# Kernel tuning notes

Measured on AMD Instinct MI355X. Metric: run time of the kernel, lower is better.

## Reference

```python
import jax, jax.numpy as jnp
import numpy as np

D_IN = 1024
D_OUT = 1024


def setup_inputs() -> dict:
    key = jax.random.key(0)
    kx, kq, kk, kv = jax.random.split(key, 4)
    x = jax.random.normal(kx, (4, 2048, D_IN), dtype=jnp.float32)
    s = 1.0 / np.sqrt(D_IN)
    Wq = jax.random.normal(kq, (D_IN, D_OUT), dtype=jnp.float32) * s
    Wk = jax.random.normal(kk, (D_IN, D_OUT), dtype=jnp.float32) * s
    Wv = jax.random.normal(kv, (D_IN, D_OUT), dtype=jnp.float32) * s
    return {"x": x, "Wq": Wq, "Wk": Wk, "Wv": Wv}


def reference(x, Wq, Wk, Wv):
    # x: [B, S, d_in]; W*: [d_in, d_out]
    B, S, _ = x.shape
    q = x @ Wq  # [B, S, d_out]
    k = x @ Wk
    v = x @ Wv
    scale = 1.0 / jnp.sqrt(jnp.asarray(k.shape[-1], x.dtype))
    scores = jnp.einsum("bqd,bkd->bqk", q, k) * scale  # [B, S, S]
    # causal mask: positions j > i masked to -inf (triu, diagonal=1)
    causal = jnp.tril(jnp.ones((S, S), dtype=bool))
    scores = jnp.where(causal[None, :, :], scores, -jnp.inf)
    attn = jax.nn.softmax(scores, axis=-1)  # dropout p=0.0 -> identity
    return jnp.einsum("bqk,bkd->bqd", attn, v)
```

## Files before the change

### kernel.cpp

```cpp
#include <hip/hip_runtime.h>
#include <hip/hip_bf16.h>

#define NB 4
#define SB 2048
#define DD 1024
#define BM 128
#define BN 128
#define BK 32

typedef __attribute__((ext_vector_type(8))) short bf16x8;
typedef __attribute__((ext_vector_type(4))) short bf16x4;
typedef __attribute__((ext_vector_type(4))) float f32x4;
typedef unsigned int u32;

__device__ __forceinline__ float bf2f(unsigned short u) {
    return __uint_as_float(((u32)u) << 16);
}
__device__ __forceinline__ short f2bf(float f) {
    u32 u = __float_as_uint(f);
    u32 r = (u + 0x7fffu + ((u >> 16) & 1u)) >> 16;
    return (short)r;
}

__device__ __forceinline__ void wait_vm8() {
    asm volatile("s_waitcnt vmcnt(8)" ::: "memory");
}
__device__ __forceinline__ void wait_vm0() {
    asm volatile("s_waitcnt vmcnt(0)" ::: "memory");
}
__device__ __forceinline__ void barrier_raw() {
    __builtin_amdgcn_s_barrier();
    asm volatile("" ::: "memory");
}

__device__ __forceinline__ void mfma_step(const short* As, const short* Bs,
                                          f32x4 (&acc)[4][4], int lane, int wave)
{
    const int wm = (wave >> 1) * 64, wn = (wave & 1) * 64;
    const int fr = lane & 15;
    const int quad = lane >> 4;
    bf16x8 af[4], bf[4];
#pragma unroll
    for (int t = 0; t < 4; t++) {
        af[t] = *(const bf16x8*)&As[(wm + t * 16 + fr) * BK + quad * 8];
        bf[t] = *(const bf16x8*)&Bs[(wn + t * 16 + fr) * BK + quad * 8];
    }
#pragma unroll
    for (int mt = 0; mt < 4; mt++)
#pragma unroll
        for (int nt = 0; nt < 4; nt++)
            acc[mt][nt] = __builtin_amdgcn_mfma_f32_16x16x32_bf16(
                af[mt], bf[nt], acc[mt][nt], 0, 0, 0);
}

__device__ __forceinline__ void mfma_step_swz(const short* As, const short* Bs,
                                              f32x4 (&acc)[4][4], int lane,
                                              int wave)
{
    const int wm = (wave >> 1) * 64, wn = (wave & 1) * 64;
    const int fr = lane & 15;
    const int qa = (lane >> 4) ^ ((fr >> 1) & 3);
    bf16x8 af[4], bf[4];
#pragma unroll
    for (int t = 0; t < 4; t++) {
        af[t] = *(const bf16x8*)&As[(wm + t * 16 + fr) * BK + qa * 8];
        bf[t] = *(const bf16x8*)&Bs[(wn + t * 16 + fr) * BK + qa * 8];
    }
#pragma unroll
    for (int mt = 0; mt < 4; mt++)
#pragma unroll
        for (int nt = 0; nt < 4; nt++)
            acc[mt][nt] = __builtin_amdgcn_mfma_f32_16x16x32_bf16(
                af[mt], bf[nt], acc[mt][nt], 0, 0, 0);
}

__device__ __forceinline__ void mfma_step_pv_swz(const short* As,
                                                 const short* Bs,
                                                 f32x4 (&acc)[2][4], int lane,
                                                 int wave)
{
    const int wm = wave * 32;
    const int fr = lane & 15;
    const int qa = (lane >> 4) ^ ((fr >> 1) & 3);
    bf16x8 af[2], bf[4];
#pragma unroll
    for (int t = 0; t < 2; t++)
        af[t] = *(const bf16x8*)&As[(wm + t * 16 + fr) * BK + qa * 8];
#pragma unroll
    for (int t = 0; t < 4; t++)
        bf[t] = *(const bf16x8*)&Bs[(t * 16 + fr) * BK + qa * 8];
#pragma unroll
    for (int mt = 0; mt < 2; mt++)
#pragma unroll
        for (int nt = 0; nt < 4; nt++)
            acc[mt][nt] = __builtin_amdgcn_mfma_f32_16x16x32_bf16(
                af[mt], bf[nt], acc[mt][nt], 0, 0, 0);
}

__device__ __forceinline__ void mfma_step256_swz(const short* As,
                                                 const short* Bs,
                                                 f32x4 (&acc)[8][4], int lane,
                                                 int wave)
{
    const int wm = (wave >> 2) * 128;
    const int wn = (wave & 3) * 64;
    const int fr = lane & 15;
    const int qa = (lane >> 4) ^ ((fr >> 1) & 3);
    bf16x8 af[8], bf[4];
#pragma unroll
    for (int t = 0; t < 8; t++)
        af[t] = *(const bf16x8*)&As[(wm + t * 16 + fr) * BK + qa * 8];
#pragma unroll
    for (int t = 0; t < 4; t++)
        bf[t] = *(const bf16x8*)&Bs[(wn + t * 16 + fr) * BK + qa * 8];
#pragma unroll
    for (int mt = 0; mt < 8; mt++)
#pragma unroll
        for (int nt = 0; nt < 4; nt++)
            acc[mt][nt] = __builtin_amdgcn_mfma_f32_16x16x32_bf16(
                af[mt], bf[nt], acc[mt][nt], 0, 0, 0);
}

__device__ __forceinline__ void stage128x32(const short* __restrict__ g, int ld,
                                            short* lds, int tid) {
    const int wave = tid >> 6, lane = tid & 63;
    const int r = lane >> 2;
    const int c = ((lane & 3) ^ ((lane >> 3) & 3)) * 8;
#pragma unroll
    for (int i = 0; i < 2; i++) {
        const int chunk = wave * 2 + i;
        const short* gp = g + (size_t)(chunk * 16 + r) * ld + c;
        __builtin_amdgcn_global_load_lds(
            (const __attribute__((address_space(1))) u32*)gp,
            (__attribute__((address_space(3))) u32*)(lds + chunk * 512 + lane * 8),
            16, 0, 0);
    }
}

__device__ __forceinline__ void stage64x32(const short* __restrict__ g, int ld,
                                           short* lds, int tid) {
    const int wave = tid >> 6, lane = tid & 63;
    const int r = lane >> 2;
    const int c = ((lane & 3) ^ ((lane >> 3) & 3)) * 8;
    const short* gp = g + (size_t)(wave * 16 + r) * ld + c;
    __builtin_amdgcn_global_load_lds(
        (const __attribute__((address_space(1))) u32*)gp,
        (__attribute__((address_space(3))) u32*)(lds + wave * 512 + lane * 8),
        16, 0, 0);
}

__device__ __forceinline__ void stage256x64(const short* __restrict__ g, int ld,
                                            short* base, int tid) {
    const int w = tid >> 6, l = tid & 63;
    const int lr = l >> 2;
    const int lc = ((l & 3) ^ ((l >> 3) & 3)) * 8;
#pragma unroll
    for (int i = 0; i < 4; i++) {
        const int ks = i >> 1;
        const int row = (i & 1) * 128 + w * 16 + lr;
        const short* gp = g + (size_t)row * ld + ks * 32 + lc;
        __builtin_amdgcn_global_load_lds(
            (const __attribute__((address_space(1))) u32*)gp,
            (__attribute__((address_space(3))) u32*)(base + i * 4096 + w * 512 + l * 8),
            16, 0, 0);
    }
}

__device__ __forceinline__ void stage_f32_128x32(const float* __restrict__ g,
                                                 int ld, short* lds, int tid) {
    const int r = tid >> 1;
    const int c = (tid & 1) * 16;
    const float* gp = &g[(size_t)r * ld + c];
    float4 v0 = *(const float4*)(gp + 0);
    float4 v1 = *(const float4*)(gp + 4);
    float4 v2 = *(const float4*)(gp + 8);
    float4 v3 = *(const float4*)(gp + 12);
    bf16x8 o0, o1;
    o0[0] = f2bf(v0.x); o0[1] = f2bf(v0.y); o0[2] = f2bf(v0.z); o0[3] = f2bf(v0.w);
    o0[4] = f2bf(v1.x); o0[5] = f2bf(v1.y); o0[6] = f2bf(v1.z); o0[7] = f2bf(v1.w);
    o1[0] = f2bf(v2.x); o1[1] = f2bf(v2.y); o1[2] = f2bf(v2.z); o1[3] = f2bf(v2.w);
    o1[4] = f2bf(v3.x); o1[5] = f2bf(v3.y); o1[6] = f2bf(v3.z); o1[7] = f2bf(v3.w);
    *(bf16x8*)&lds[r * BK + c] = o0;
    *(bf16x8*)&lds[r * BK + c + 8] = o1;
}

__global__ __launch_bounds__(256) void prep_mm(
    const float* __restrict__ x, const float* __restrict__ Wq,
    const float* __restrict__ Wk, const float* __restrict__ Wv,
    short* __restrict__ xb, short* __restrict__ Wvt, float* __restrict__ Mp4)
{
    __shared__ short As[BM * BK], Bs[BN * BK];
    __shared__ short t[64][65];
    const int bx = blockIdx.x;
    const int tid = threadIdx.x;
    if (bx < 256) {
        const int ch = bx >> 6;
        const int t64 = bx & 63;
        const int m0 = (t64 >> 3) * BM;
        const int n0 = (t64 & 7) * BN;
        const int kbase = ch * 256;
        const int lane = tid & 63, wave = tid >> 6;
        f32x4 acc[4][4];
#pragma unroll
        for (int a = 0; a < 4; a++)
#pragma unroll
            for (int b = 0; b < 4; b++) acc[a][b] = (f32x4){0.f, 0.f, 0.f, 0.f};
        for (int k0 = 0; k0 < 256; k0 += BK) {
            stage_f32_128x32(Wk + (size_t)m0 * DD + kbase + k0, DD, As, tid);
            stage_f32_128x32(Wq + (size_t)n0 * DD + kbase + k0, DD, Bs, tid);
            __syncthreads();
            mfma_step(As, Bs, acc, lane, wave);
            __syncthreads();
        }
        const int wm = (wave >> 1) * 64, wn = (wave & 1) * 64;
        const int fr = lane & 15, quad = lane >> 4;
        float* Mc = Mp4 + (size_t)ch * DD * DD;
#pragma unroll
        for (int mt = 0; mt < 4; mt++)
#pragma unroll
            for (int nt = 0; nt < 4; nt++)
#pragma unroll
                for (int r = 0; r < 4; r++) {
                    const size_t m = m0 + wm + mt * 16 + quad * 4 + r;
                    const size_t n = n0 + wn + nt * 16 + fr;
                    Mc[m * DD + n] = acc[mt][nt][r];
                }
        return;
    }
    if (bx < 4352) {
        const size_t i = ((size_t)(bx - 256) * 256 + tid) * 8;
        float4 a = *(const float4*)&x[i];
        float4 b = *(const float4*)&x[i + 4];
        bf16x8 o;
        o[0] = f2bf(a.x); o[1] = f2bf(a.y); o[2] = f2bf(a.z); o[3] = f2bf(a.w);
        o[4] = f2bf(b.x); o[5] = f2bf(b.y); o[6] = f2bf(b.z); o[7] = f2bf(b.w);
        *(bf16x8*)&xb[i] = o;
        return;
    }
    const int rr = bx - 4352;
    const int k0 = (rr & 15) * 64;
    const int n0 = (rr >> 4) * 64;
    {
        const int r = tid >> 4;
        const int c = (tid & 15) * 4;
#pragma unroll
        for (int i = 0; i < 4; i++) {
            float4 v = *(const float4*)&Wv[(size_t)(k0 + i * 16 + r) * DD + n0 + c];
            t[i * 16 + r][c + 0] = f2bf(v.x);
            t[i * 16 + r][c + 1] = f2bf(v.y);
            t[i * 16 + r][c + 2] = f2bf(v.z);
            t[i * 16 + r][c + 3] = f2bf(v.w);
        }
    }
    __syncthreads();
    {
        const int r = tid >> 3;
        const int c = (tid & 7) * 8;
#pragma unroll
        for (int i = 0; i < 2; i++) {
            bf16x8 o;
#pragma unroll
            for (int j = 0; j < 8; j++) o[j] = t[c + j][i * 32 + r];
            *(bf16x8*)&Wvt[(size_t)(n0 + i * 32 + r) * DD + k0 + c] = o;
        }
    }
}

__global__ __launch_bounds__(256) void mm_reduce(const float* __restrict__ Mp4,
                                                 short* __restrict__ Mp)
{
    const size_t e = ((size_t)blockIdx.x * 256 + threadIdx.x) * 4;
    const size_t N = (size_t)DD * DD;
    float4 s = *(const float4*)&Mp4[e];
#pragma unroll
    for (int c = 1; c < 4; c++) {
        float4 p = *(const float4*)&Mp4[c * N + e];
        s.x += p.x; s.y += p.y; s.z += p.z; s.w += p.w;
    }
    bf16x4 o;
    o[0] = f2bf(s.x); o[1] = f2bf(s.y); o[2] = f2bf(s.z); o[3] = f2bf(s.w);
    *(bf16x4*)&Mp[e] = o;
}

__global__ __launch_bounds__(512) void tv_gemm(
    const short* __restrict__ xb, const short* __restrict__ Mp,
    const short* __restrict__ Wvt, short* __restrict__ T,
    short* __restrict__ Vt)
{
    __shared__ short lds[2 * 32768];
    const int lin = blockIdx.x + 4 * blockIdx.y;
    const int swz = (lin & 7) * 16 + (lin >> 3);
    const int n0 = (swz & 3) * 256;
    const int m0 = (swz >> 2) * 256;
    const int isv = blockIdx.z;
    const short* Bt = isv ? Wvt : Mp;
    const short* Ap = xb + (size_t)m0 * DD;
    const short* Bp = Bt + (size_t)n0 * DD;
    const int tid = threadIdx.x;
    const int lane = tid & 63, wave = tid >> 6;
    f32x4 acc[8][4];
#pragma unroll
    for (int a = 0; a < 8; a++)
#pragma unroll
        for (int b = 0; b < 4; b++) acc[a][b] = (f32x4){0.f, 0.f, 0.f, 0.f};

    stage256x64(Ap, DD, lds, tid);
    stage256x64(Bp, DD, lds + 16384, tid);
    for (int j = 0; j < 16; ++j) {
        const int cur = j & 1;
        short* slot = lds + cur * 32768;
        if (j < 15) {
            short* nxt = lds + (cur ^ 1) * 32768;
            stage256x64(Ap + (j + 1) * 64, DD, nxt, tid);
            stage256x64(Bp + (j + 1) * 64, DD, nxt + 16384, tid);
            wait_vm8();
        } else {
            wait_vm0();
        }
        barrier_raw();
        __builtin_amdgcn_s_setprio(1);
        mfma_step256_swz(slot, slot + 16384, acc, lane, wave);
        mfma_step256_swz(slot + 8192, slot + 16384 + 8192, acc, lane, wave);
        __builtin_amdgcn_s_setprio(0);
        barrier_raw();
    }

    const int wm = (wave >> 2) * 128, wn = (wave & 3) * 64;
    const int fr = lane & 15, quad = lane >> 4;
    if (!isv) {
#pragma unroll
        for (int mt = 0; mt < 8; mt++)
#pragma unroll
            for (int nt = 0; nt < 4; nt++)
#pragma unroll
                for (int r = 0; r < 4; r++) {
                    const size_t m = m0 + wm + mt * 16 + quad * 4 + r;
                    const size_t n = n0 + wn + nt * 16 + fr;
                    T[m * DD + n] = f2bf(acc[mt][nt][r]);
                }
    } else {
        const int bb = m0 >> 11;
        const int s0 = (m0 & (SB - 1)) + wm + quad * 4;
        short* Vb = Vt + (size_t)bb * DD * SB;
#pragma unroll
        for (int mt = 0; mt < 8; mt++)
#pragma unroll
            for (int nt = 0; nt < 4; nt++) {
                const size_t n = n0 + wn + nt * 16 + fr;
                const size_t s = s0 + mt * 16;
                bf16x4 o;
#pragma unroll
                for (int r = 0; r < 4; r++) o[r] = f2bf(acc[mt][nt][r]);
                *(bf16x4*)&Vb[n * SB + s] = o;
            }
    }
}

__global__ __launch_bounds__(256) void scores_mfma(
    const short* __restrict__ T, const short* __restrict__ xb,
    short* __restrict__ Sc)
{
    const int bx = blockIdx.x;
    const int idx = (bx & 7) * 34 + (bx >> 3);
    int qt = (int)((__fsqrt_rn(4.f * idx + 1.f) - 1.f) * 0.5f);
    while ((qt + 1) * (qt + 2) <= idx) qt++;
    while (qt * (qt + 1) > idx) qt--;
    const int kt = idx - qt * (qt + 1);
    const int qm0 = qt * BM;
    const int kn0 = kt * 64;
    const int b = blockIdx.y;
    __shared__ short As[2 * BM * BK], Bs[2 * 64 * BK];
    const short* Tq = T + (size_t)b * SB * DD + (size_t)qm0 * DD;
    const short* Xk = xb + (size_t)b * SB * DD + (size_t)kn0 * DD;
    short* Sb = Sc + (size_t)b * SB * SB;
    const int tid = threadIdx.x;
    const int lane = tid & 63, wave = tid >> 6;
    f32x4 acc[2][4];
#pragma unroll
    for (int a = 0; a < 2; a++)
#pragma unroll
        for (int c = 0; c < 4; c++) acc[a][c] = (f32x4){0.f, 0.f, 0.f, 0.f};
    for (int k0 = 0; k0 < DD; k0 += 2 * BK) {
        stage128x32(Tq + k0, DD, As, tid);
        stage128x32(Tq + k0 + BK, DD, As + BM * BK, tid);
        stage64x32(Xk + k0, DD, Bs, tid);
        stage64x32(Xk + k0 + BK, DD, Bs + 64 * BK, tid);
        __syncthreads();
        mfma_step_pv_swz(As, Bs, acc, lane, wave);
        mfma_step_pv_swz(As + BM * BK, Bs + 64 * BK, acc, lane, wave);
        __syncthreads();
    }
    const int fr = lane & 15, quad = lane >> 4;
    const float scale = 0.03125f;
#pragma unroll
    for (int mt = 0; mt < 2; mt++)
#pragma unroll
        for (int nt = 0; nt < 4; nt++)
#pragma unroll
            for (int r = 0; r < 4; r++) {
                const size_t q = qm0 + wave * 32 + mt * 16 + quad * 4 + r;
                const size_t k = kn0 + nt * 16 + fr;
                Sb[q * SB + k] = f2bf(acc[mt][nt][r] * scale);
            }
}

__global__ __launch_bounds__(256) void softmax_kernel(short* __restrict__ Sc)
{
    const int row = blockIdx.x;
    const int i = row & (SB - 1);
    const int jlim = ((i >> 7) + 1) << 7;
    short* r = Sc + (size_t)row * SB;
    const int t = threadIdx.x;
    const int lane = t & 63, wave = t >> 6;
    __shared__ float red[8];

    const int j0 = t * 8;
    bf16x8 in = {0, 0, 0, 0, 0, 0, 0, 0};
    if (j0 <= i) in = *(const bf16x8*)&r[j0];
    float v[8];
    float mx = -1e30f;
#pragma unroll
    for (int e = 0; e < 8; e++) {
        const float s = (j0 + e <= i) ? bf2f((unsigned short)in[e]) : -1e30f;
        v[e] = s;
        mx = fmaxf(mx, s);
    }
#pragma unroll
    for (int o = 32; o > 0; o >>= 1) mx = fmaxf(mx, __shfl_down(mx, o));
    if (lane == 0) red[wave] = mx;
    __syncthreads();
    mx = fmaxf(fmaxf(red[0], red[1]), fmaxf(red[2], red[3]));

    float sum = 0.f;
#pragma unroll
    for (int e = 0; e < 8; e++) {
        const float x = (j0 + e <= i) ? __expf(v[e] - mx) : 0.f;
        v[e] = x;
        sum += x;
    }
#pragma unroll
    for (int o = 32; o > 0; o >>= 1) sum += __shfl_down(sum, o);
    if (lane == 0) red[4 + wave] = sum;
    __syncthreads();
    const float inv = 1.0f / (red[4] + red[5] + red[6] + red[7]);
    if (j0 < jlim) {
        bf16x8 o;
#pragma unroll
        for (int e = 0; e < 8; e++) o[e] = f2bf(v[e] * inv);
        *(bf16x8*)&r[j0] = o;
    }
}

__global__ __launch_bounds__(256) void pv_mfma(
    const short* __restrict__ P, const short* __restrict__ Vt,
    float* __restrict__ O)
{
    __shared__ short As[2 * 8192], Bs[2 * 8192];
    const int pair = blockIdx.x;
    const int n0 = blockIdx.y * 128;
    const int b = blockIdx.z;
    const short* Pb = P + (size_t)b * SB * SB;
    const short* Vb = Vt + (size_t)b * DD * SB;
    float* Ob = O + (size_t)b * SB * DD;
    const int tid = threadIdx.x;
    const int lane = tid & 63, wave = tid >> 6;
    const int fr = lane & 15, quad = lane >> 4;
    for (int half = 0; half < 2; ++half) {
        const int qt = half ? (15 - pair) : pair;
        const int qm0 = qt * BM;
        const int nj = (qt + 1) * 2;
        const short* Pq = Pb + (size_t)qm0 * SB;
        const short* Vn = Vb + (size_t)n0 * SB;
        f32x4 acc[4][4];
#pragma unroll
        for (int a = 0; a < 4; a++)
#pragma unroll
            for (int c = 0; c < 4; c++) acc[a][c] = (f32x4){0.f, 0.f, 0.f, 0.f};
        stage128x32(Pq, SB, As, tid);
        stage128x32(Pq + BK, SB, As + 4096, tid);
        stage128x32(Vn, SB, Bs, tid);
        stage128x32(Vn + BK, SB, Bs + 4096, tid);
        for (int j = 0; j < nj; ++j) {
            const int cur = j & 1;
            const short* as = As + cur * 8192;
            const short* bs = Bs + cur * 8192;
            if (j + 1 < nj) {
                const int off = (j + 1) * 64;
                short* an = As + (cur ^ 1) * 8192;
                short* bn = Bs + (cur ^ 1) * 8192;
                stage128x32(Pq + off, SB, an, tid);
                stage128x32(Pq + off + BK, SB, an + 4096, tid);
                stage128x32(Vn + off, SB, bn, tid);
                stage128x32(Vn + off + BK, SB, bn + 4096, tid);
                wait_vm8();
            } else {
                wait_vm0();
            }
            barrier_raw();
            __builtin_amdgcn_s_setprio(1);
            mfma_step_swz(as, bs, acc, lane, wave);
            mfma_step_swz(as + 4096, bs + 4096, acc, lane, wave);
            __builtin_amdgcn_s_setprio(0);
            barrier_raw();
        }
        const int wm = (wave >> 1) * 64, wn = (wave & 1) * 64;
#pragma unroll
        for (int mt = 0; mt < 4; mt++)
#pragma unroll
            for (int nt = 0; nt < 4; nt++)
#pragma unroll
                for (int r = 0; r < 4; r++) {
                    const size_t q = qm0 + wm + mt * 16 + quad * 4 + r;
                    const size_t n = n0 + wn + nt * 16 + fr;
                    Ob[q * DD + n] = acc[mt][nt][r];
                }
    }
}

extern "C" void kernel_launch(void* const* d_in, const int* in_sizes, int n_in,
                              void* d_out, int out_size, void* d_ws, size_t ws_size,
                              hipStream_t stream)
{
    const float* x  = (const float*)d_in[0];
    const float* Wq = (const float*)d_in[1];
    const float* Wk = (const float*)d_in[2];
    const float* Wv = (const float*)d_in[3];
    float* out = (float*)d_out;

    const size_t XE = (size_t)NB * SB * DD;
    const size_t WE = (size_t)DD * DD;
    short* xb  = (short*)d_ws;
    short* T   = xb + XE;
    short* Vt  = T + XE;
    short* Sc  = Vt + XE;
    float* Pp  = (float*)(Sc + (size_t)NB * SB * SB);
    short* Wvt = (short*)(Pp + (size_t)NB * 1024 * DD);
    short* Mp  = Wvt + WE;
    float* Mp4 = (float*)Sc;

    prep_mm<<<dim3(256 + 4096 + 256), 256, 0, stream>>>(
        x, Wq, Wk, Wv, xb, Wvt, Mp4);
    mm_reduce<<<dim3(1024), 256, 0, stream>>>(Mp4, Mp);
    tv_gemm<<<dim3(4, 32, 2), 512, 0, stream>>>(xb, Mp, Wvt, T, Vt);
    scores_mfma<<<dim3(272, NB), 256, 0, stream>>>(T, xb, Sc);
    softmax_kernel<<<dim3(NB * SB), 256, 0, stream>>>(Sc);
    pv_mfma<<<dim3(8, 8, NB), 256, 0, stream>>>(Sc, Vt, out);
}
```

Baseline: 227.9 us.

## Use 128x128 tiles with double-buffered async staging in causal scores kernel

The scores kernel moves from 128x64 tiles over the lower-triangular block layout to 128x128 tiles, halving the grid and increasing reuse of each staged tile. It also replaces the synchronous load-then-compute loop with a double-buffered pipeline that prefetches the next 64-wide K slice while MFMAs run, using vmcnt waits, raw barriers and setprio. The cost is more LDS (64 KB) and more accumulator registers per block, plus fewer blocks to fill the machine. Diagonal tiles now compute a full 128x128 block, but the 128-aligned row limit in softmax already accounts for that.

```diff
diff --git a/kernel.cpp b/kernel.cpp
--- a/kernel.cpp
+++ b/kernel.cpp
@@ -68,29 +68,6 @@
     }
 #pragma unroll
     for (int mt = 0; mt < 4; mt++)
-#pragma unroll
-        for (int nt = 0; nt < 4; nt++)
-            acc[mt][nt] = __builtin_amdgcn_mfma_f32_16x16x32_bf16(
-                af[mt], bf[nt], acc[mt][nt], 0, 0, 0);
-}
-
-__device__ __forceinline__ void mfma_step_pv_swz(const short* As,
-                                                 const short* Bs,
-                                                 f32x4 (&acc)[2][4], int lane,
-                                                 int wave)
-{
-    const int wm = wave * 32;
-    const int fr = lane & 15;
-    const int qa = (lane >> 4) ^ ((fr >> 1) & 3);
-    bf16x8 af[2], bf[4];
-#pragma unroll
-    for (int t = 0; t < 2; t++)
-        af[t] = *(const bf16x8*)&As[(wm + t * 16 + fr) * BK + qa * 8];
-#pragma unroll
-    for (int t = 0; t < 4; t++)
-        bf[t] = *(const bf16x8*)&Bs[(t * 16 + fr) * BK + qa * 8];
-#pragma unroll
-    for (int mt = 0; mt < 2; mt++)
 #pragma unroll
         for (int nt = 0; nt < 4; nt++)
             acc[mt][nt] = __builtin_amdgcn_mfma_f32_16x16x32_bf16(
@@ -135,18 +112,6 @@
             (__attribute__((address_space(3))) u32*)(lds + chunk * 512 + lane * 8),
             16, 0, 0);
     }
-}
-
-__device__ __forceinline__ void stage64x32(const short* __restrict__ g, int ld,
-                                           short* lds, int tid) {
-    const int wave = tid >> 6, lane = tid & 63;
-    const int r = lane >> 2;
-    const int c = ((lane & 3) ^ ((lane >> 3) & 3)) * 8;
-    const short* gp = g + (size_t)(wave * 16 + r) * ld + c;
-    __builtin_amdgcn_global_load_lds(
-        (const __attribute__((address_space(1))) u32*)gp,
-        (__attribute__((address_space(3))) u32*)(lds + wave * 512 + lane * 8),
-        16, 0, 0);
 }
 
 __device__ __forceinline__ void stage256x64(const short* __restrict__ g, int ld,
@@ -360,46 +325,64 @@
     const short* __restrict__ T, const short* __restrict__ xb,
     short* __restrict__ Sc)
 {
+    __shared__ short As[2 * 8192], Bs[2 * 8192];
     const int bx = blockIdx.x;
-    const int idx = (bx & 7) * 34 + (bx >> 3);
-    int qt = (int)((__fsqrt_rn(4.f * idx + 1.f) - 1.f) * 0.5f);
-    while ((qt + 1) * (qt + 2) <= idx) qt++;
-    while (qt * (qt + 1) > idx) qt--;
-    const int kt = idx - qt * (qt + 1);
+    const int idx = (bx & 7) * 17 + (bx >> 3);
+    int qt = (int)((__fsqrt_rn(8.f * idx + 1.f) - 1.f) * 0.5f);
+    while ((qt + 1) * (qt + 2) / 2 <= idx) qt++;
+    while (qt * (qt + 1) / 2 > idx) qt--;
+    const int kt = idx - qt * (qt + 1) / 2;
     const int qm0 = qt * BM;
-    const int kn0 = kt * 64;
+    const int kn0 = kt * BN;
     const int b = blockIdx.y;
-    __shared__ short As[2 * BM * BK], Bs[2 * 64 * BK];
     const short* Tq = T + (size_t)b * SB * DD + (size_t)qm0 * DD;
     const short* Xk = xb + (size_t)b * SB * DD + (size_t)kn0 * DD;
     short* Sb = Sc + (size_t)b * SB * SB;
     const int tid = threadIdx.x;
     const int lane = tid & 63, wave = tid >> 6;
-    f32x4 acc[2][4];
-#pragma unroll
-    for (int a = 0; a < 2; a++)
+    f32x4 acc[4][4];
+#pragma unroll
+    for (int a = 0; a < 4; a++)
 #pragma unroll
         for (int c = 0; c < 4; c++) acc[a][c] = (f32x4){0.f, 0.f, 0.f, 0.f};
-    for (int k0 = 0; k0 < DD; k0 += 2 * BK) {
-        stage128x32(Tq + k0, DD, As, tid);
-        stage128x32(Tq + k0 + BK, DD, As + BM * BK, tid);
-        stage64x32(Xk + k0, DD, Bs, tid);
-        stage64x32(Xk + k0 + BK, DD, Bs + 64 * BK, tid);
-        __syncthreads();
-        mfma_step_pv_swz(As, Bs, acc, lane, wave);
-        mfma_step_pv_swz(As + BM * BK, Bs + 64 * BK, acc, lane, wave);
-        __syncthreads();
-    }
+    stage128x32(Tq, DD, As, tid);
+    stage128x32(Tq + BK, DD, As + 4096, tid);
+    stage128x32(Xk, DD, Bs, tid);
+    stage128x32(Xk + BK, DD, Bs + 4096, tid);
+    for (int j = 0; j < 16; ++j) {
+        const int cur = j & 1;
+        const short* as = As + cur * 8192;
+        const short* bs = Bs + cur * 8192;
+        if (j < 15) {
+            const int off = (j + 1) * 64;
+            short* an = As + (cur ^ 1) * 8192;
+            short* bn = Bs + (cur ^ 1) * 8192;
+            stage128x32(Tq + off, DD, an, tid);
+            stage128x32(Tq + off + BK, DD, an + 4096, tid);
+            stage128x32(Xk + off, DD, bn, tid);
+            stage128x32(Xk + off + BK, DD, bn + 4096, tid);
+            wait_vm8();
+        } else {
+            wait_vm0();
+        }
+        barrier_raw();
+        __builtin_amdgcn_s_setprio(1);
+        mfma_step_swz(as, bs, acc, lane, wave);
+        mfma_step_swz(as + 4096, bs + 4096, acc, lane, wave);
+        __builtin_amdgcn_s_setprio(0);
+        barrier_raw();
+    }
+    const int wm = (wave >> 1) * 64, wn = (wave & 1) * 64;
     const int fr = lane & 15, quad = lane >> 4;
     const float scale = 0.03125f;
 #pragma unroll
-    for (int mt = 0; mt < 2; mt++)
+    for (int mt = 0; mt < 4; mt++)
 #pragma unroll
         for (int nt = 0; nt < 4; nt++)
 #pragma unroll
             for (int r = 0; r < 4; r++) {
-                const size_t q = qm0 + wave * 32 + mt * 16 + quad * 4 + r;
-                const size_t k = kn0 + nt * 16 + fr;
+                const size_t q = qm0 + wm + mt * 16 + quad * 4 + r;
+                const size_t k = kn0 + wn + nt * 16 + fr;
                 Sb[q * SB + k] = f2bf(acc[mt][nt][r] * scale);
             }
 }
@@ -542,7 +525,7 @@
         x, Wq, Wk, Wv, xb, Wvt, Mp4);
     mm_reduce<<<dim3(1024), 256, 0, stream>>>(Mp4, Mp);
     tv_gemm<<<dim3(4, 32, 2), 512, 0, stream>>>(xb, Mp, Wvt, T, Vt);
-    scores_mfma<<<dim3(272, NB), 256, 0, stream>>>(T, xb, Sc);
+    scores_mfma<<<dim3(136, NB), 256, 0, stream>>>(T, xb, Sc);
     softmax_kernel<<<dim3(NB * SB), 256, 0, stream>>>(Sc);
     pv_mfma<<<dim3(8, 8, NB), 256, 0, stream>>>(Sc, Vt, out);
 }
```

Measured after the change: 237.2 us. 1.04x slower.

## Drop split-K for Wk·Wqᵀ product and remove separate reduction kernel

Applied to the files above, without the earlier changes.

The Wk·Wqᵀ matrix product is now computed by 64 blocks each covering the full K range, instead of 256 blocks splitting K in four and writing fp32 partials. Each block stages two 32-wide K slices per sync and writes bf16 output directly. This removes the mm_reduce launch and the fp32 partial traffic. The cost is fewer, longer blocks on the critical path of prep_mm, which lowers parallelism for that part while the conversion blocks run alongside.

```diff
diff --git a/kernel.cpp b/kernel.cpp
--- a/kernel.cpp
+++ b/kernel.cpp
@@ -187,34 +187,33 @@
 __global__ __launch_bounds__(256) void prep_mm(
     const float* __restrict__ x, const float* __restrict__ Wq,
     const float* __restrict__ Wk, const float* __restrict__ Wv,
-    short* __restrict__ xb, short* __restrict__ Wvt, float* __restrict__ Mp4)
-{
-    __shared__ short As[BM * BK], Bs[BN * BK];
+    short* __restrict__ xb, short* __restrict__ Wvt, short* __restrict__ Mp)
+{
+    __shared__ short As[2 * BM * BK], Bs[2 * BN * BK];
     __shared__ short t[64][65];
     const int bx = blockIdx.x;
     const int tid = threadIdx.x;
-    if (bx < 256) {
-        const int ch = bx >> 6;
-        const int t64 = bx & 63;
-        const int m0 = (t64 >> 3) * BM;
-        const int n0 = (t64 & 7) * BN;
-        const int kbase = ch * 256;
+    if (bx < 64) {
+        const int m0 = (bx >> 3) * BM;
+        const int n0 = (bx & 7) * BN;
         const int lane = tid & 63, wave = tid >> 6;
         f32x4 acc[4][4];
 #pragma unroll
         for (int a = 0; a < 4; a++)
 #pragma unroll
             for (int b = 0; b < 4; b++) acc[a][b] = (f32x4){0.f, 0.f, 0.f, 0.f};
-        for (int k0 = 0; k0 < 256; k0 += BK) {
-            stage_f32_128x32(Wk + (size_t)m0 * DD + kbase + k0, DD, As, tid);
-            stage_f32_128x32(Wq + (size_t)n0 * DD + kbase + k0, DD, Bs, tid);
+        for (int k0 = 0; k0 < DD; k0 += 2 * BK) {
+            stage_f32_128x32(Wk + (size_t)m0 * DD + k0, DD, As, tid);
+            stage_f32_128x32(Wk + (size_t)m0 * DD + k0 + BK, DD, As + 4096, tid);
+            stage_f32_128x32(Wq + (size_t)n0 * DD + k0, DD, Bs, tid);
+            stage_f32_128x32(Wq + (size_t)n0 * DD + k0 + BK, DD, Bs + 4096, tid);
             __syncthreads();
             mfma_step(As, Bs, acc, lane, wave);
+            mfma_step(As + 4096, Bs + 4096, acc, lane, wave);
             __syncthreads();
         }
         const int wm = (wave >> 1) * 64, wn = (wave & 1) * 64;
         const int fr = lane & 15, quad = lane >> 4;
-        float* Mc = Mp4 + (size_t)ch * DD * DD;
 #pragma unroll
         for (int mt = 0; mt < 4; mt++)
 #pragma unroll
@@ -223,12 +222,12 @@
                 for (int r = 0; r < 4; r++) {
                     const size_t m = m0 + wm + mt * 16 + quad * 4 + r;
                     const size_t n = n0 + wn + nt * 16 + fr;
-                    Mc[m * DD + n] = acc[mt][nt][r];
+                    Mp[m * DD + n] = f2bf(acc[mt][nt][r]);
                 }
         return;
     }
-    if (bx < 4352) {
-        const size_t i = ((size_t)(bx - 256) * 256 + tid) * 8;
+    if (bx < 4160) {
+        const size_t i = ((size_t)(bx - 64) * 256 + tid) * 8;
         float4 a = *(const float4*)&x[i];
         float4 b = *(const float4*)&x[i + 4];
         bf16x8 o;
@@ -237,7 +236,7 @@
         *(bf16x8*)&xb[i] = o;
         return;
     }
-    const int rr = bx - 4352;
+    const int rr = bx - 4160;
     const int k0 = (rr & 15) * 64;
     const int n0 = (rr >> 4) * 64;
     {
@@ -264,22 +263,6 @@
             *(bf16x8*)&Wvt[(size_t)(n0 + i * 32 + r) * DD + k0 + c] = o;
         }
     }
-}
-
-__global__ __launch_bounds__(256) void mm_reduce(const float* __restrict__ Mp4,
-                                                 short* __restrict__ Mp)
-{
-    const size_t e = ((size_t)blockIdx.x * 256 + threadIdx.x) * 4;
-    const size_t N = (size_t)DD * DD;
-    float4 s = *(const float4*)&Mp4[e];
-#pragma unroll
-    for (int c = 1; c < 4; c++) {
-        float4 p = *(const float4*)&Mp4[c * N + e];
-        s.x += p.x; s.y += p.y; s.z += p.z; s.w += p.w;
-    }
-    bf16x4 o;
-    o[0] = f2bf(s.x); o[1] = f2bf(s.y); o[2] = f2bf(s.z); o[3] = f2bf(s.w);
-    *(bf16x4*)&Mp[e] = o;
 }
 
 __global__ __launch_bounds__(512) void tv_gemm(
@@ -536,11 +519,9 @@
     float* Pp  = (float*)(Sc + (size_t)NB * SB * SB);
     short* Wvt = (short*)(Pp + (size_t)NB * 1024 * DD);
     short* Mp  = Wvt + WE;
-    float* Mp4 = (float*)Sc;
-
-    prep_mm<<<dim3(256 + 4096 + 256), 256, 0, stream>>>(
-        x, Wq, Wk, Wv, xb, Wvt, Mp4);
-    mm_reduce<<<dim3(1024), 256, 0, stream>>>(Mp4, Mp);
+
+    prep_mm<<<dim3(64 + 4096 + 256), 256, 0, stream>>>(
+        x, Wq, Wk, Wv, xb, Wvt, Mp);
     tv_gemm<<<dim3(4, 32, 2), 512, 0, stream>>>(xb, Mp, Wvt, T, Vt);
     scores_mfma<<<dim3(272, NB), 256, 0, stream>>>(T, xb, Sc);
     softmax_kernel<<<dim3(NB * SB), 256, 0, stream>>>(Sc);
```

Result: slower. 238.9 us (+4.8%).
